# Kernel optimization log

Hardware: AMD Instinct MI355X
Metric: run time of the kernel (lower is better)

The kernel has to match this reference:

```python
import jax, jax.numpy as jnp
import numpy as np

EMBED_DIM = 1024
SEQ_LEN = 2048
BATCH = 4


def setup_inputs() -> dict:
    key = jax.random.key(0)
    kx, kq, kk, kv = jax.random.split(key, 4)
    scale = 1.0 / np.sqrt(EMBED_DIM)
    x = jax.random.normal(kx, (BATCH, SEQ_LEN, EMBED_DIM), dtype=jnp.float32)
    # nn.Linear weights are [out, in]; stored transposed-application here
    W_query = jax.random.normal(kq, (EMBED_DIM, EMBED_DIM), dtype=jnp.float32) * scale
    W_key = jax.random.normal(kk, (EMBED_DIM, EMBED_DIM), dtype=jnp.float32) * scale
    W_value = jax.random.normal(kv, (EMBED_DIM, EMBED_DIM), dtype=jnp.float32) * scale
    return {"x": x, "W_query": W_query, "W_key": W_key, "W_value": W_value}


def reference(x, W_query, W_key, W_value):
    # x: [B, S, D]; W_*: [D_out, D_in] (torch nn.Linear layout -> y = x @ W.T)
    B, S, D = x.shape
    q = jnp.einsum("bsd,ed->bse", x, W_query)
    k = jnp.einsum("bsd,ed->bse", x, W_key)
    v = jnp.einsum("bsd,ed->bse", x, W_value)
    scores = jnp.einsum("bqd,bkd->bqk", q, k)  # [B, S, S]
    causal = jnp.triu(jnp.ones((S, S), dtype=bool), k=1)  # True above diagonal
    scores = jnp.where(causal, -jnp.inf, scores)
    weights = jax.nn.softmax(scores / jnp.sqrt(jnp.asarray(D, x.dtype)), axis=-1)
    return jnp.einsum("bqk,bkd->bqd", weights, v)
```

## Files before the change

### kernel.cpp

```cpp
#include <hip/hip_runtime.h>
#include <stdint.h>

typedef __bf16 bf16_t;
typedef __bf16 bf16x4 __attribute__((ext_vector_type(4)));
typedef __bf16 bf16x8 __attribute__((ext_vector_type(8)));
typedef float  f32x4  __attribute__((ext_vector_type(4)));

#define AS1 __attribute__((address_space(1)))
#define AS3 __attribute__((address_space(3)))

__device__ __forceinline__ void gld_lds16(const bf16_t* g, void* s) {
  __builtin_amdgcn_global_load_lds((const AS1 uint32_t*)g, (AS3 uint32_t*)s, 16, 0, 0);
}

__global__ __launch_bounds__(256) void convert_all_kernel(
    const float* __restrict__ X,  const float* __restrict__ Wq,
    const float* __restrict__ Wk, const float* __restrict__ Wv,
    bf16_t* __restrict__ Xc, bf16_t* __restrict__ Wqc,
    bf16_t* __restrict__ Wkc, bf16_t* __restrict__ Wvc) {
  const int blk = blockIdx.x;
  const float* src; bf16_t* dst; int base;
  if (blk < 4096)      { src = X;  dst = Xc;  base = 0;    }
  else if (blk < 4608) { src = Wq; dst = Wqc; base = 4096; }
  else if (blk < 5120) { src = Wk; dst = Wkc; base = 4608; }
  else                 { src = Wv; dst = Wvc; base = 5120; }
  const int i = ((blk - base) * 256 + threadIdx.x) * 8;
  const float4 a = ((const float4*)(src + i))[0];
  const float4 b = ((const float4*)(src + i))[1];
  bf16x8 v;
  v[0] = (bf16_t)a.x; v[1] = (bf16_t)a.y; v[2] = (bf16_t)a.z; v[3] = (bf16_t)a.w;
  v[4] = (bf16_t)b.x; v[5] = (bf16_t)b.y; v[6] = (bf16_t)b.z; v[7] = (bf16_t)b.w;
  *(bf16x8*)(dst + i) = v;
}

__device__ __forceinline__ void gemm_thin_core(
    const bf16_t* __restrict__ A, int lda,
    const bf16_t* __restrict__ B, int ldb,
    int m0, int n0, int kEnd,
    char* lds, f32x4 acc[4][4])
{
  const int tid  = threadIdx.x;
  const int lane = tid & 63;
  const int wave = tid >> 6;
  const int wm = (wave >> 2) * 64;
  const int wn = (wave & 3) * 64;
  const int fr = lane & 15;
  const int ck = lane >> 4;

  const int srow = tid >> 2;
  const int sch  = tid & 3;
  const int kg   = (sch ^ (srow & 3)) * 8;
  const int dstA = srow * 64 + sch * 16;
  const int dstB = dstA;

  const bf16_t* Ar  = A + (size_t)(m0 + srow) * lda + kg;
  const bf16_t* Br0 = B + (size_t)(n0 + srow) * ldb + kg;
  const bf16_t* Br1 = B + (size_t)(n0 + srow + 128) * ldb + kg;

  int aoff[4], boff[4];
#pragma unroll
  for (int i = 0; i < 4; ++i) {
    const int ra = wm + i * 16 + fr;
    const int rb = wn + i * 16 + fr;
    aoff[i] = ra * 64 + ((ck ^ (ra & 3)) * 16);
    boff[i] = rb * 64 + ((ck ^ (rb & 3)) * 16);
  }

  gld_lds16(Ar, lds + dstA);
  gld_lds16(Br0, lds + 16384 + dstB);
  gld_lds16(Br1, lds + 16384 + 8192 + dstB);

  const int NK = kEnd >> 5;
  int cur = 0;
  for (int t = 0; t < NK; ++t) {
    const int nxt = cur ^ 1;
    if (t + 1 < NK) {
      const int ko = (t + 1) * 32;
      gld_lds16(Ar + ko, lds + nxt * 8192 + dstA);
      gld_lds16(Br0 + ko, lds + 16384 + nxt * 16384 + dstB);
      gld_lds16(Br1 + ko, lds + 16384 + nxt * 16384 + 8192 + dstB);
      asm volatile("s_waitcnt vmcnt(3)" ::: "memory");
    } else {
      asm volatile("s_waitcnt vmcnt(0)" ::: "memory");
    }
    __builtin_amdgcn_sched_barrier(0);
    __builtin_amdgcn_s_barrier();
    __builtin_amdgcn_sched_barrier(0);

    const char* Ab = lds + cur * 8192;
    const char* Bb = lds + 16384 + cur * 16384;
    bf16x8 af[4], bfv[4];
#pragma unroll
    for (int i = 0; i < 4; ++i) {
      af[i]  = *(const bf16x8*)(Ab + aoff[i]);
      bfv[i] = *(const bf16x8*)(Bb + boff[i]);
    }
    asm volatile("s_waitcnt lgkmcnt(0)" ::: "memory");
    __builtin_amdgcn_sched_barrier(0);
    __builtin_amdgcn_s_setprio(1);
#pragma unroll
    for (int mi = 0; mi < 4; ++mi)
#pragma unroll
      for (int ni = 0; ni < 4; ++ni)
        acc[mi][ni] = __builtin_amdgcn_mfma_f32_16x16x32_bf16(
            af[mi], bfv[ni], acc[mi][ni], 0, 0, 0);
    __builtin_amdgcn_s_setprio(0);
    __builtin_amdgcn_sched_barrier(0);
    __builtin_amdgcn_s_barrier();
    __builtin_amdgcn_sched_barrier(0);
    cur = nxt;
  }
}

__device__ __forceinline__ void gemm256_core(
    const bf16_t* __restrict__ A, int lda,
    const bf16_t* __restrict__ B, int ldb,
    int m0, int n0, int kEnd,
    char* lds, f32x4 acc[8][4])
{
  const int tid  = threadIdx.x;
  const int lane = tid & 63;
  const int wave = tid >> 6;
  const int wm = (wave >> 2) * 128;
  const int wn = (wave & 3) * 64;
  const int fr = lane & 15;
  const int ck = lane >> 4;

  const int srow = tid >> 3;
  const int sch  = tid & 7;
  const int kgs  = (sch ^ (srow & 7)) * 8;
  const int sdst = srow * 128 + sch * 16;

  const bf16_t* Ar = A + (size_t)(m0 + srow) * lda + kgs;
  const bf16_t* Br = B + (size_t)(n0 + srow) * ldb + kgs;

  int aoffs[8], boffs[4];
#pragma unroll
  for (int mi = 0; mi < 8; ++mi) {
    const int ra = wm + mi * 16 + fr;
    aoffs[mi] = ra * 128 + ((ck ^ (ra & 7)) * 16);
  }
#pragma unroll
  for (int ni = 0; ni < 4; ++ni) {
    const int rb = wn + ni * 16 + fr;
    boffs[ni] = rb * 128 + ((ck ^ (rb & 7)) * 16);
  }

#pragma unroll
  for (int j = 0; j < 4; ++j) {
    gld_lds16(Ar + (size_t)(j * 64) * lda, lds + j * 8192 + sdst);
    gld_lds16(Br + (size_t)(j * 64) * ldb, lds + 65536 + j * 8192 + sdst);
  }

  const int NK = kEnd >> 6;
  int cur = 0;
  for (int t = 0; t < NK; ++t) {
    const int nxt = cur ^ 1;
    if (t + 1 < NK) {
      const bf16_t* An = Ar + (t + 1) * 64;
      const bf16_t* Bn = Br + (t + 1) * 64;
#pragma unroll
      for (int j = 0; j < 4; ++j) {
        gld_lds16(An + (size_t)(j * 64) * lda, lds + nxt * 32768 + j * 8192 + sdst);
        gld_lds16(Bn + (size_t)(j * 64) * ldb, lds + 65536 + nxt * 32768 + j * 8192 + sdst);
      }
      asm volatile("s_waitcnt vmcnt(8)" ::: "memory");
    } else {
      asm volatile("s_waitcnt vmcnt(0)" ::: "memory");
    }
    __builtin_amdgcn_sched_barrier(0);
    __builtin_amdgcn_s_barrier();
    __builtin_amdgcn_sched_barrier(0);

    const char* Ab = lds + cur * 32768;
    const char* Bb = lds + 65536 + cur * 32768;
#pragma unroll
    for (int ks = 0; ks < 2; ++ks) {
      bf16x8 af[8], bfv[4];
#pragma unroll
      for (int mi = 0; mi < 8; ++mi)
        af[mi] = *(const bf16x8*)(Ab + (aoffs[mi] ^ (ks * 64)));
#pragma unroll
      for (int ni = 0; ni < 4; ++ni)
        bfv[ni] = *(const bf16x8*)(Bb + (boffs[ni] ^ (ks * 64)));
      asm volatile("s_waitcnt lgkmcnt(0)" ::: "memory");
      __builtin_amdgcn_sched_barrier(0);
      __builtin_amdgcn_s_setprio(1);
#pragma unroll
      for (int mi = 0; mi < 8; ++mi)
#pragma unroll
        for (int ni = 0; ni < 4; ++ni)
          acc[mi][ni] = __builtin_amdgcn_mfma_f32_16x16x32_bf16(
              af[mi], bfv[ni], acc[mi][ni], 0, 0, 0);
      __builtin_amdgcn_s_setprio(0);
    }
    asm volatile("s_waitcnt lgkmcnt(0)" ::: "memory");
    __builtin_amdgcn_sched_barrier(0);
    __builtin_amdgcn_s_barrier();
    __builtin_amdgcn_sched_barrier(0);
    cur = nxt;
  }
}

__device__ __forceinline__ void gemm_bt_core(
    const bf16_t* __restrict__ A, int lda,
    const bf16_t* __restrict__ B, int ldb,
    int m0, int n0, int kBeg, int kEnd,
    bf16_t* As, bf16_t* Bs, f32x4 acc[4][4])
{
  const int lane = threadIdx.x & 63;
  const int wave = threadIdx.x >> 6;
  const int wm = (wave >> 1) * 64;
  const int wn = (wave & 1) * 64;
  const int fr = lane & 15;
  const int ck = lane >> 4;

  const int off0 = wave * 2048 + lane * 16;
  const int row0 = wave * 32 + (lane >> 2);
  const int row1 = row0 + 16;
  const int kg   = ((lane & 3) ^ ((row0 >> 1) & 3)) * 8;

  const bf16_t* Ar0 = A + (size_t)(m0 + row0) * lda + kg;
  const bf16_t* Ar1 = A + (size_t)(m0 + row1) * lda + kg;
  const bf16_t* Br0 = B + (size_t)(n0 + row0) * ldb + kg;
  const bf16_t* Br1 = B + (size_t)(n0 + row1) * ldb + kg;

  int aoff[4], boff[4];
#pragma unroll
  for (int i = 0; i < 4; ++i) {
    const int ra = wm + i * 16 + fr;
    const int rb = wn + i * 16 + fr;
    aoff[i] = ra * 64 + ((ck ^ ((ra >> 1) & 3)) * 16);
    boff[i] = rb * 64 + ((ck ^ ((rb >> 1) & 3)) * 16);
  }

  gld_lds16(Ar0 + kBeg, (char*)As + off0);
  gld_lds16(Ar1 + kBeg, (char*)As + off0 + 1024);
  gld_lds16(Br0 + kBeg, (char*)Bs + off0);
  gld_lds16(Br1 + kBeg, (char*)Bs + off0 + 1024);

  int cur = 0;
  for (int kt = kBeg; kt < kEnd; kt += 32) {
    const int nxt = cur ^ 1;
    if (kt + 32 < kEnd) {
      gld_lds16(Ar0 + kt + 32, (char*)As + nxt * 8192 + off0);
      gld_lds16(Ar1 + kt + 32, (char*)As + nxt * 8192 + off0 + 1024);
      gld_lds16(Br0 + kt + 32, (char*)Bs + nxt * 8192 + off0);
      gld_lds16(Br1 + kt + 32, (char*)Bs + nxt * 8192 + off0 + 1024);
      asm volatile("s_waitcnt vmcnt(4)" ::: "memory");
    } else {
      asm volatile("s_waitcnt vmcnt(0)" ::: "memory");
    }
    __builtin_amdgcn_sched_barrier(0);
    __builtin_amdgcn_s_barrier();
    __builtin_amdgcn_sched_barrier(0);

    bf16x8 af[4], bfv[4];
#pragma unroll
    for (int mi = 0; mi < 4; ++mi)
      af[mi] = *(const bf16x8*)((char*)As + cur * 8192 + aoff[mi]);
#pragma unroll
    for (int ni = 0; ni < 4; ++ni)
      bfv[ni] = *(const bf16x8*)((char*)Bs + cur * 8192 + boff[ni]);
    __builtin_amdgcn_s_setprio(1);
#pragma unroll
    for (int mi = 0; mi < 4; ++mi)
#pragma unroll
      for (int ni = 0; ni < 4; ++ni)
        acc[mi][ni] = __builtin_amdgcn_mfma_f32_16x16x32_bf16(
            af[mi], bfv[ni], acc[mi][ni], 0, 0, 0);
    __builtin_amdgcn_s_setprio(0);

    asm volatile("s_waitcnt lgkmcnt(0)" ::: "memory");
    __builtin_amdgcn_sched_barrier(0);
    __builtin_amdgcn_s_barrier();
    __builtin_amdgcn_sched_barrier(0);
    cur = nxt;
  }
}

__global__ __launch_bounds__(512) void qkv_kernel(
    const bf16_t* __restrict__ X,
    const bf16_t* __restrict__ Wq, const bf16_t* __restrict__ Wk,
    const bf16_t* __restrict__ Wv,
    bf16_t* __restrict__ Q, bf16_t* __restrict__ K, bf16_t* __restrict__ Vt)
{
  __shared__ bf16_t smem[24576];
  const int bid = blockIdx.x;
  const int z   = bid >> 8;
  const int t   = bid & 255;
  const int m0  = (t >> 2) * 128;
  const int n0  = (t & 3) * 256;
  const bf16_t* W = (z == 0) ? Wq : (z == 1) ? Wk : Wv;

  f32x4 acc[4][4] = {};
  gemm_thin_core(X, 1024, W, 1024, m0, n0, 1024, (char*)smem, acc);

  const int tid  = threadIdx.x;
  const int lane = tid & 63;
  const int wave = tid >> 6;
  const int wm = (wave >> 2) * 64, wn = (wave & 3) * 64;

  if (z < 2) {
    bf16_t* Out = z ? K : Q;
#pragma unroll
    for (int mi = 0; mi < 4; ++mi)
#pragma unroll
      for (int r = 0; r < 4; ++r) {
        const int row = m0 + wm + mi * 16 + (lane >> 4) * 4 + r;
#pragma unroll
        for (int ni = 0; ni < 4; ++ni) {
          const int col = n0 + wn + ni * 16 + (lane & 15);
          Out[(size_t)row * 1024 + col] = (bf16_t)acc[mi][ni][r];
        }
      }
  } else {
    const int b  = m0 >> 11;
    const int s0 = m0 & 2047;
    bf16_t* Vtb = Vt + (size_t)b * 1024 * 2048;
    bf16_t (*tb)[136] = (bf16_t(*)[136])smem;
#pragma unroll
    for (int h = 0; h < 4; ++h) {
      __syncthreads();
      if ((wave & 3) == h) {
#pragma unroll
        for (int mi = 0; mi < 4; ++mi)
#pragma unroll
          for (int ni = 0; ni < 4; ++ni) {
            const int c    = ni * 16 + (lane & 15);
            const int rowl = wm + mi * 16 + (lane >> 4) * 4;
            bf16x4 v;
            v[0] = (bf16_t)acc[mi][ni][0]; v[1] = (bf16_t)acc[mi][ni][1];
            v[2] = (bf16_t)acc[mi][ni][2]; v[3] = (bf16_t)acc[mi][ni][3];
            *(bf16x4*)&tb[c][rowl] = v;
          }
      }
      __syncthreads();
#pragma unroll
      for (int i = 0; i < 2; ++i) {
        const int idx = tid + 512 * i;
        const int d   = idx >> 4;
        const int ch  = idx & 15;
        bf16x8 vv = *(const bf16x8*)&tb[d][ch * 8];
        *(bf16x8*)(Vtb + (size_t)(n0 + h * 64 + d) * 2048 + s0 + ch * 8) = vv;
      }
    }
  }
}

__global__ __launch_bounds__(512) void scores_exp_kernel(
    const bf16_t* __restrict__ Q, const bf16_t* __restrict__ K,
    bf16_t* __restrict__ P, float* __restrict__ partials)
{
  const int kt = blockIdx.x;
  const int mt = blockIdx.y;
  if (kt > mt) return;
  const int m0 = mt * 256;
  const int n0 = kt * 256;
  __shared__ bf16_t smem[65536];
  const int batch = blockIdx.z;
  const bf16_t* Qb = Q + (size_t)batch * 2048 * 1024;
  const bf16_t* Kb = K + (size_t)batch * 2048 * 1024;
  bf16_t* Pb = P + (size_t)batch * 2048 * 2048;
  float* lp  = partials + (size_t)batch * 16 * 2048;

  f32x4 acc[8][4] = {};
  gemm256_core(Qb, 1024, Kb, 1024, m0, n0, 1024, (char*)smem, acc);

  const int tid  = threadIdx.x;
  const int lane = tid & 63;
  const int wave = tid >> 6;
  const int wm = (wave >> 2) * 128, wn = (wave & 3) * 64;
  float (*rowsum)[256] = (float(*)[256])smem;
  const float c = 0.04508422f;
#pragma unroll
  for (int mi = 0; mi < 8; ++mi)
#pragma unroll
    for (int r = 0; r < 4; ++r) {
      const int lrow = wm + mi * 16 + (lane >> 4) * 4 + r;
      const int row  = m0 + lrow;
      float rs = 0.f;
#pragma unroll
      for (int ni = 0; ni < 4; ++ni) {
        const int col = n0 + wn + ni * 16 + (lane & 15);
        float p = exp2f(acc[mi][ni][r] * c);
        if (col > row) p = 0.f;
        const bf16_t pb = (bf16_t)p;
        Pb[(size_t)row * 2048 + col] = pb;
        rs += (float)pb;
      }
      rs += __shfl_xor(rs, 1);
      rs += __shfl_xor(rs, 2);
      rs += __shfl_xor(rs, 4);
      rs += __shfl_xor(rs, 8);
      if ((lane & 15) == 0) rowsum[wave & 3][lrow] = rs;
    }
  __syncthreads();
  {
    const int row = tid & 255;
    const int s   = tid >> 8;
    lp[(size_t)(2 * kt + s) * 2048 + m0 + row] =
        rowsum[2 * s][row] + rowsum[2 * s + 1][row];
  }
}

__global__ __launch_bounds__(256) void lsum_kernel(
    const float* __restrict__ partials, float* __restrict__ Linv)
{
  const int id  = blockIdx.x * 256 + threadIdx.x;
  const int z   = id >> 11;
  const int row = id & 2047;
  const float* lp = partials + (size_t)z * 16 * 2048;
  const int tmax = row >> 7;
  float l = 0.f;
  for (int kt = 0; kt <= tmax; ++kt) l += lp[kt * 2048 + row];
  Linv[id] = 1.f / l;
}

__global__ __launch_bounds__(256) void pv_kernel(
    const bf16_t* __restrict__ P, const bf16_t* __restrict__ Vt,
    const float* __restrict__ Linv, float* __restrict__ out)
{
  __shared__ bf16_t smem[4 * 128 * 32];
  bf16_t* As = smem;
  bf16_t* Bs = smem + 2 * 128 * 32;
  const int zb = blockIdx.z;
  const int mt = ((zb >> 1) & 1) ? (15 - blockIdx.y) : blockIdx.y;
  const int m0 = mt * 128;
  const int n0 = blockIdx.x * 128;
  const bf16_t* Pb  = P  + (size_t)zb * 2048 * 2048;
  const bf16_t* Vtb = Vt + (size_t)zb * 1024 * 2048;
  const float* li = Linv + (size_t)zb * 2048;
  float* ob = out + (size_t)zb * 2048 * 1024;

  f32x4 acc[4][4] = {};
  gemm_bt_core(Pb, 2048, Vtb, 2048, m0, n0, 0, m0 + 128, As, Bs, acc);

  const int lane = threadIdx.x & 63;
  const int wave = threadIdx.x >> 6;
  const int wm = (wave >> 1) * 64, wn = (wave & 1) * 64;
#pragma unroll
  for (int mi = 0; mi < 4; ++mi)
#pragma unroll
    for (int r = 0; r < 4; ++r) {
      const int row = m0 + wm + mi * 16 + (lane >> 4) * 4 + r;
      const float inv = li[row];
#pragma unroll
      for (int ni = 0; ni < 2; ++ni) {
        const int col = n0 + wn + ni * 16 + (lane & 15);
        ob[(size_t)row * 1024 + col] = acc[mi][ni][r] * inv;
      }
#pragma unroll
      for (int ni = 2; ni < 4; ++ni) {
        const int col = n0 + wn + ni * 16 + (lane & 15);
        ob[(size_t)row * 1024 + col] = acc[mi][ni][r] * inv;
      }
    }
}

extern "C" void kernel_launch(void* const* d_in, const int* in_sizes, int n_in,
                              void* d_out, int out_size, void* d_ws, size_t ws_size,
                              hipStream_t stream) {
  const float* X  = (const float*)d_in[0];
  const float* Wq = (const float*)d_in[1];
  const float* Wk = (const float*)d_in[2];
  const float* Wv = (const float*)d_in[3];
  float* out = (float*)d_out;
  char* ws = (char*)d_ws;

  const size_t MB = 1024 * 1024;
  bf16_t* Q    = (bf16_t*)(ws + 0 * MB);
  bf16_t* K    = (bf16_t*)(ws + 16 * MB);
  bf16_t* Vt   = (bf16_t*)(ws + 32 * MB);
  bf16_t* Xc   = (bf16_t*)(ws + 48 * MB);
  bf16_t* Wqc  = (bf16_t*)(ws + 64 * MB);
  bf16_t* Wkc  = (bf16_t*)(ws + 66 * MB);
  bf16_t* Wvc  = (bf16_t*)(ws + 68 * MB);
  bf16_t* P    = (bf16_t*)(ws + 48 * MB);
  float*  Lp   = (float*)(ws + 80 * MB);
  float*  Linv = (float*)(ws + 80 * MB + 512 * 1024);

  convert_all_kernel<<<dim3(5632), 256, 0, stream>>>(X, Wq, Wk, Wv, Xc, Wqc, Wkc, Wvc);
  qkv_kernel<<<dim3(768), 512, 0, stream>>>(Xc, Wqc, Wkc, Wvc, Q, K, Vt);
  scores_exp_kernel<<<dim3(8, 8, 4), 512, 0, stream>>>(Q, K, P, Lp);
  lsum_kernel<<<dim3(32), 256, 0, stream>>>(Lp, Linv);
  pv_kernel<<<dim3(8, 16, 4), 256, 0, stream>>>(P, Vt, Linv, out);
}
```

Baseline: 231.5 us.

## Use 128x256 thin-tile GEMM core for causal scores kernel

The scores kernel moves from the 256x256 gemm256_core to the existing 128x256 gemm_thin_core, so the grid goes from 8x8 to 8x16 row tiles per batch. This gives more active blocks, less wasted work above the causal diagonal at finer granularity, and a much smaller LDS footprint, which should raise occupancy. The thin core's LDS swizzle is also changed to use (row>>1)&3 to cut bank conflicts. The trade-off is less data reuse per block and more redundant K loads.

```diff
diff --git a/kernel.cpp b/kernel.cpp
--- a/kernel.cpp
+++ b/kernel.cpp
@@ -49,7 +49,7 @@
 
   const int srow = tid >> 2;
   const int sch  = tid & 3;
-  const int kg   = (sch ^ (srow & 3)) * 8;
+  const int kg   = (sch ^ ((srow >> 1) & 3)) * 8;
   const int dstA = srow * 64 + sch * 16;
   const int dstB = dstA;
 
@@ -62,8 +62,8 @@
   for (int i = 0; i < 4; ++i) {
     const int ra = wm + i * 16 + fr;
     const int rb = wn + i * 16 + fr;
-    aoff[i] = ra * 64 + ((ck ^ (ra & 3)) * 16);
-    boff[i] = rb * 64 + ((ck ^ (rb & 3)) * 16);
+    aoff[i] = ra * 64 + ((ck ^ ((ra >> 1) & 3)) * 16);
+    boff[i] = rb * 64 + ((ck ^ ((rb >> 1) & 3)) * 16);
   }
 
   gld_lds16(Ar, lds + dstA);
@@ -112,96 +112,6 @@
   }
 }
 
-__device__ __forceinline__ void gemm256_core(
-    const bf16_t* __restrict__ A, int lda,
-    const bf16_t* __restrict__ B, int ldb,
-    int m0, int n0, int kEnd,
-    char* lds, f32x4 acc[8][4])
-{
-  const int tid  = threadIdx.x;
-  const int lane = tid & 63;
-  const int wave = tid >> 6;
-  const int wm = (wave >> 2) * 128;
-  const int wn = (wave & 3) * 64;
-  const int fr = lane & 15;
-  const int ck = lane >> 4;
-
-  const int srow = tid >> 3;
-  const int sch  = tid & 7;
-  const int kgs  = (sch ^ (srow & 7)) * 8;
-  const int sdst = srow * 128 + sch * 16;
-
-  const bf16_t* Ar = A + (size_t)(m0 + srow) * lda + kgs;
-  const bf16_t* Br = B + (size_t)(n0 + srow) * ldb + kgs;
-
-  int aoffs[8], boffs[4];
-#pragma unroll
-  for (int mi = 0; mi < 8; ++mi) {
-    const int ra = wm + mi * 16 + fr;
-    aoffs[mi] = ra * 128 + ((ck ^ (ra & 7)) * 16);
-  }
-#pragma unroll
-  for (int ni = 0; ni < 4; ++ni) {
-    const int rb = wn + ni * 16 + fr;
-    boffs[ni] = rb * 128 + ((ck ^ (rb & 7)) * 16);
-  }
-
-#pragma unroll
-  for (int j = 0; j < 4; ++j) {
-    gld_lds16(Ar + (size_t)(j * 64) * lda, lds + j * 8192 + sdst);
-    gld_lds16(Br + (size_t)(j * 64) * ldb, lds + 65536 + j * 8192 + sdst);
-  }
-
-  const int NK = kEnd >> 6;
-  int cur = 0;
-  for (int t = 0; t < NK; ++t) {
-    const int nxt = cur ^ 1;
-    if (t + 1 < NK) {
-      const bf16_t* An = Ar + (t + 1) * 64;
-      const bf16_t* Bn = Br + (t + 1) * 64;
-#pragma unroll
-      for (int j = 0; j < 4; ++j) {
-        gld_lds16(An + (size_t)(j * 64) * lda, lds + nxt * 32768 + j * 8192 + sdst);
-        gld_lds16(Bn + (size_t)(j * 64) * ldb, lds + 65536 + nxt * 32768 + j * 8192 + sdst);
-      }
-      asm volatile("s_waitcnt vmcnt(8)" ::: "memory");
-    } else {
-      asm volatile("s_waitcnt vmcnt(0)" ::: "memory");
-    }
-    __builtin_amdgcn_sched_barrier(0);
-    __builtin_amdgcn_s_barrier();
-    __builtin_amdgcn_sched_barrier(0);
-
-    const char* Ab = lds + cur * 32768;
-    const char* Bb = lds + 65536 + cur * 32768;
-#pragma unroll
-    for (int ks = 0; ks < 2; ++ks) {
-      bf16x8 af[8], bfv[4];
-#pragma unroll
-      for (int mi = 0; mi < 8; ++mi)
-        af[mi] = *(const bf16x8*)(Ab + (aoffs[mi] ^ (ks * 64)));
-#pragma unroll
-      for (int ni = 0; ni < 4; ++ni)
-        bfv[ni] = *(const bf16x8*)(Bb + (boffs[ni] ^ (ks * 64)));
-      asm volatile("s_waitcnt lgkmcnt(0)" ::: "memory");
-      __builtin_amdgcn_sched_barrier(0);
-      __builtin_amdgcn_s_setprio(1);
-#pragma unroll
-      for (int mi = 0; mi < 8; ++mi)
-#pragma unroll
-        for (int ni = 0; ni < 4; ++ni)
-          acc[mi][ni] = __builtin_amdgcn_mfma_f32_16x16x32_bf16(
-              af[mi], bfv[ni], acc[mi][ni], 0, 0, 0);
-      __builtin_amdgcn_s_setprio(0);
-    }
-    asm volatile("s_waitcnt lgkmcnt(0)" ::: "memory");
-    __builtin_amdgcn_sched_barrier(0);
-    __builtin_amdgcn_s_barrier();
-    __builtin_amdgcn_sched_barrier(0);
-    cur = nxt;
-  }
-}
-
 __device__ __forceinline__ void gemm_bt_core(
     const bf16_t* __restrict__ A, int lda,
     const bf16_t* __restrict__ B, int ldb,
@@ -352,29 +262,29 @@
     const bf16_t* __restrict__ Q, const bf16_t* __restrict__ K,
     bf16_t* __restrict__ P, float* __restrict__ partials)
 {
-  const int kt = blockIdx.x;
+  const int nt = blockIdx.x;
   const int mt = blockIdx.y;
-  if (kt > mt) return;
-  const int m0 = mt * 256;
-  const int n0 = kt * 256;
-  __shared__ bf16_t smem[65536];
+  if (nt > (mt >> 1)) return;
+  const int m0 = mt * 128;
+  const int n0 = nt * 256;
+  __shared__ bf16_t smem[24576];
   const int batch = blockIdx.z;
   const bf16_t* Qb = Q + (size_t)batch * 2048 * 1024;
   const bf16_t* Kb = K + (size_t)batch * 2048 * 1024;
   bf16_t* Pb = P + (size_t)batch * 2048 * 2048;
   float* lp  = partials + (size_t)batch * 16 * 2048;
 
-  f32x4 acc[8][4] = {};
-  gemm256_core(Qb, 1024, Kb, 1024, m0, n0, 1024, (char*)smem, acc);
+  f32x4 acc[4][4] = {};
+  gemm_thin_core(Qb, 1024, Kb, 1024, m0, n0, 1024, (char*)smem, acc);
 
   const int tid  = threadIdx.x;
   const int lane = tid & 63;
   const int wave = tid >> 6;
-  const int wm = (wave >> 2) * 128, wn = (wave & 3) * 64;
-  float (*rowsum)[256] = (float(*)[256])smem;
+  const int wm = (wave >> 2) * 64, wn = (wave & 3) * 64;
+  float (*rs4)[128] = (float(*)[128])smem;
   const float c = 0.04508422f;
 #pragma unroll
-  for (int mi = 0; mi < 8; ++mi)
+  for (int mi = 0; mi < 4; ++mi)
 #pragma unroll
     for (int r = 0; r < 4; ++r) {
       const int lrow = wm + mi * 16 + (lane >> 4) * 4 + r;
@@ -393,14 +303,14 @@
       rs += __shfl_xor(rs, 2);
       rs += __shfl_xor(rs, 4);
       rs += __shfl_xor(rs, 8);
-      if ((lane & 15) == 0) rowsum[wave & 3][lrow] = rs;
+      if ((lane & 15) == 0) rs4[wave & 3][lrow] = rs;
     }
   __syncthreads();
-  {
-    const int row = tid & 255;
-    const int s   = tid >> 8;
-    lp[(size_t)(2 * kt + s) * 2048 + m0 + row] =
-        rowsum[2 * s][row] + rowsum[2 * s + 1][row];
+  if (tid < 256) {
+    const int row = tid & 127;
+    const int s   = tid >> 7;
+    lp[(size_t)(2 * nt + s) * 2048 + m0 + row] =
+        rs4[2 * s][row] + rs4[2 * s + 1][row];
   }
 }
 
@@ -446,12 +356,7 @@
       const int row = m0 + wm + mi * 16 + (lane >> 4) * 4 + r;
       const float inv = li[row];
 #pragma unroll
-      for (int ni = 0; ni < 2; ++ni) {
-        const int col = n0 + wn + ni * 16 + (lane & 15);
-        ob[(size_t)row * 1024 + col] = acc[mi][ni][r] * inv;
-      }
-#pragma unroll
-      for (int ni = 2; ni < 4; ++ni) {
+      for (int ni = 0; ni < 4; ++ni) {
         const int col = n0 + wn + ni * 16 + (lane & 15);
         ob[(size_t)row * 1024 + col] = acc[mi][ni][r] * inv;
       }
@@ -482,7 +387,7 @@
 
   convert_all_kernel<<<dim3(5632), 256, 0, stream>>>(X, Wq, Wk, Wv, Xc, Wqc, Wkc, Wvc);
   qkv_kernel<<<dim3(768), 512, 0, stream>>>(Xc, Wqc, Wkc, Wvc, Q, K, Vt);
-  scores_exp_kernel<<<dim3(8, 8, 4), 512, 0, stream>>>(Q, K, P, Lp);
+  scores_exp_kernel<<<dim3(8, 16, 4), 512, 0, stream>>>(Q, K, P, Lp);
   lsum_kernel<<<dim3(32), 256, 0, stream>>>(Lp, Linv);
   pv_kernel<<<dim3(8, 16, 4), 256, 0, stream>>>(P, Vt, Linv, out);
 }
```

Measured after the change: 225.3 us. 2.7% less time.
